# Kernel optimization log

Hardware: AMD Instinct MI355X
Metric: run time of the kernel (lower is better)

The kernel has to match this reference:

```python
import jax, jax.numpy as jnp
import numpy as np

B, P, D, H = 4, 2048, 768, 12
DFF = 4 * D
EPS = 1e-3  # Keras LayerNormalization default epsilon
SURVIVAL_PROB = 0.9  # inference-mode droppath scaling


def setup_inputs() -> dict:
    key = jax.random.key(0)
    ks = jax.random.split(key, 4)
    s = 0.02
    return {
        "x": jax.random.normal(ks[0], (B, P, D), dtype=jnp.float32),
        "ln1_g": jnp.ones((D,), jnp.float32),
        "ln1_b": jnp.zeros((D,), jnp.float32),
        "w_qkv": jax.random.normal(ks[1], (D, 3 * D), jnp.float32) * s,
        "b_qkv": jnp.zeros((3 * D,), jnp.float32),
        "ln2_g": jnp.ones((D,), jnp.float32),
        "ln2_b": jnp.zeros((D,), jnp.float32),
        "w1": jax.random.normal(ks[2], (D, DFF), jnp.float32) * s,
        "b1": jnp.zeros((DFF,), jnp.float32),
        "w2": jax.random.normal(ks[3], (DFF, D), jnp.float32) * s,
        "b2": jnp.zeros((D,), jnp.float32),
    }


def _layernorm(x, g, b):
    mu = jnp.mean(x, axis=-1, keepdims=True)
    var = jnp.mean(jnp.square(x - mu), axis=-1, keepdims=True)
    return (x - mu) * jax.lax.rsqrt(var + EPS) * g + b


def _block(x, ln1_g, ln1_b, w_qkv, b_qkv, ln2_g, ln2_b, w1, b1, w2, b2):
    # --- pre-norm self-attention ---
    h = _layernorm(x, ln1_g, ln1_b)
    qkv = h @ w_qkv + b_qkv                      # [B,P,3D]
    q, k, v = jnp.split(qkv, 3, axis=-1)
    hd = D // H
    to_heads = lambda t: t.reshape(B, P, H, hd).transpose(0, 2, 1, 3)  # b h p c
    q, k, v = to_heads(q), to_heads(k), to_heads(v)
    scale = jnp.sqrt(jnp.float32(D / H))
    scores = jnp.einsum('bhqc,bhkc->bhqk', q, k) / scale
    attn = jax.nn.softmax(scores, axis=-1)
    o = jnp.einsum('bhqk,bhkc->bhqc', attn, v)
    o = o.transpose(0, 2, 1, 3).reshape(B, P, D)
    x = o * SURVIVAL_PROB + x
    # --- pre-norm MLP ---
    h = _layernorm(x, ln2_g, ln2_b)
    h = jax.nn.gelu(h @ w1 + b1, approximate=False)
    h = h @ w2 + b2
    return h * SURVIVAL_PROB + x


def reference(x, ln1_g, ln1_b, w_qkv, b_qkv, ln2_g, ln2_b, w1, b1, w2, b2):
    return _block(x, ln1_g, ln1_b, w_qkv, b_qkv, ln2_g, ln2_b, w1, b1, w2, b2)
```

## Files before the change

kernel.cpp:

```cpp
#include <hip/hip_runtime.h>
#include <hip/hip_bf16.h>
#include <math.h>

#define B_ 4
#define P_ 2048
#define D_ 768
#define H_ 12

typedef __attribute__((ext_vector_type(8))) short bf16x8;
typedef __attribute__((ext_vector_type(4))) float f32x4;

static __device__ __forceinline__ short f2bf(float f) {
  union { float f; unsigned u; } z; z.f = f;
  unsigned r = z.u + 0x7fffu + ((z.u >> 16) & 1u);
  return (short)(r >> 16);
}

static __device__ __forceinline__ float bf2f(short s) {
  union { unsigned u; float f; } z;
  z.u = ((unsigned)(unsigned short)s) << 16;
  return z.f;
}

static __device__ __forceinline__ void gll16(const void* g, void* l) {
  __builtin_amdgcn_global_load_lds(
      (const __attribute__((address_space(1))) void*)g,
      (__attribute__((address_space(3))) void*)l, 16, 0, 0);
}

static __device__ __forceinline__ int vswz(int d) {
  return ((d & 7) ^ ((d >> 3) & 7)) << 3;
}

__global__ __launch_bounds__(256) void tcvt_kernel(const float* __restrict__ in,
                                                   short* __restrict__ out, int K, int N) {
  __shared__ float t[32][33];
  int k0 = blockIdx.x * 32, n0 = blockIdx.y * 32;
  int tx = threadIdx.x & 31, ty = threadIdx.x >> 5;
#pragma unroll
  for (int i = 0; i < 4; ++i)
    t[ty + 8 * i][tx] = in[(size_t)(k0 + ty + 8 * i) * N + n0 + tx];
  __syncthreads();
#pragma unroll
  for (int i = 0; i < 4; ++i)
    out[(size_t)(n0 + ty + 8 * i) * K + k0 + tx] = f2bf(t[tx][ty + 8 * i]);
}

__global__ __launch_bounds__(256) void ln_kernel(const float* __restrict__ in,
                                                 const float* __restrict__ g,
                                                 const float* __restrict__ be,
                                                 short* __restrict__ out) {
  int row = blockIdx.x, tid = threadIdx.x;
  const float* xr = in + (size_t)row * D_;
  float v0 = xr[tid], v1 = xr[tid + 256], v2 = xr[tid + 512];
  float s = v0 + v1 + v2;
  float ss = v0 * v0 + v1 * v1 + v2 * v2;
#pragma unroll
  for (int d = 1; d < 64; d <<= 1) {
    s += __shfl_xor(s, d, 64);
    ss += __shfl_xor(ss, d, 64);
  }
  __shared__ float red[8];
  int w = tid >> 6;
  if ((tid & 63) == 0) { red[w] = s; red[4 + w] = ss; }
  __syncthreads();
  s = red[0] + red[1] + red[2] + red[3];
  ss = red[4] + red[5] + red[6] + red[7];
  float mu = s * (1.0f / D_);
  float rstd = rsqrtf(ss * (1.0f / D_) - mu * mu + 1e-3f);
  short* orow = out + (size_t)row * D_;
  orow[tid]       = f2bf((v0 - mu) * rstd * g[tid]       + be[tid]);
  orow[tid + 256] = f2bf((v1 - mu) * rstd * g[tid + 256] + be[tid + 256]);
  orow[tid + 512] = f2bf((v2 - mu) * rstd * g[tid + 512] + be[tid + 512]);
}

template <int EPI>
__global__ __launch_bounds__(256, 3) void gemm128(
    const short* __restrict__ A, const short* __restrict__ Bt,
    const float* __restrict__ bias, short* __restrict__ out_bf,
    float* __restrict__ out_f, const float* __restrict__ resid,
    int M, int N, int K) {
  alignas(16) __shared__ short a_lds[128 * 32];
  alignas(16) __shared__ short b_lds[128 * 32];
  const int tid = threadIdx.x;
  const int wv = tid >> 6, lane = tid & 63;
  const int wm = wv >> 1, wn = wv & 1;
  const int g = lane >> 4, r = lane & 15;
  const int m0 = blockIdx.x * 128, n0 = blockIdx.y * 128;
  const int srow = lane >> 2, sseg = lane & 3;
  f32x4 acc[4][4] = {};
  const short* aptr = A + (size_t)(m0 + wv * 16 + srow) * K + sseg * 8;
  const short* bptr = Bt + (size_t)(n0 + wv * 16 + srow) * K + sseg * 8;
  short* alds0 = &a_lds[(wv * 16) * 32];
  short* blds0 = &b_lds[(wv * 16) * 32];
  for (int k0 = 0; k0 < K; k0 += 32) {
    __syncthreads();
    gll16(aptr + k0, alds0);
    gll16(aptr + k0 + (size_t)64 * K, alds0 + 64 * 32);
    gll16(bptr + k0, blds0);
    gll16(bptr + k0 + (size_t)64 * K, blds0 + 64 * 32);
    __syncthreads();
    bf16x8 af[4], bfr[4];
#pragma unroll
    for (int i = 0; i < 4; ++i)
      af[i] = *reinterpret_cast<const bf16x8*>(&a_lds[(wm * 64 + i * 16 + r) * 32 + g * 8]);
#pragma unroll
    for (int i = 0; i < 4; ++i)
      bfr[i] = *reinterpret_cast<const bf16x8*>(&b_lds[(wn * 64 + i * 16 + r) * 32 + g * 8]);
#pragma unroll
    for (int i = 0; i < 4; ++i)
#pragma unroll
      for (int jn = 0; jn < 4; ++jn)
        acc[i][jn] = __builtin_amdgcn_mfma_f32_16x16x32_bf16(af[i], bfr[jn], acc[i][jn], 0, 0, 0);
  }
#pragma unroll
  for (int i = 0; i < 4; ++i) {
#pragma unroll
    for (int jn = 0; jn < 4; ++jn) {
      int col = n0 + wn * 64 + jn * 16 + r;
      float bb = bias[col];
#pragma unroll
      for (int jj = 0; jj < 4; ++jj) {
        int row = m0 + wm * 64 + i * 16 + g * 4 + jj;
        float v = acc[i][jn][jj] + bb;
        size_t idx = (size_t)row * N + col;
        if (EPI == 0) {
          out_bf[idx] = f2bf(v);
        } else if (EPI == 1) {
          v = 0.5f * v * (1.0f + erff(v * 0.70710678118654752f));
          out_bf[idx] = f2bf(v);
        } else {
          out_f[idx] = v * 0.9f + resid[idx];
        }
      }
    }
  }
}

__global__ __launch_bounds__(256, 3) void attn_kernel(const short* __restrict__ qkv,
                                                      const float* __restrict__ x,
                                                      float* __restrict__ x2) {
  alignas(16) __shared__ short k_lds[64 * 72];
  alignas(16) __shared__ short vt_lds[64 * 64];
  alignas(16) __shared__ short p_lds[4][32 * 72];
  const int tid = threadIdx.x, wv = tid >> 6, lane = tid & 63;
  const int g = lane >> 4, r = lane & 15;
  const int b = blockIdx.y / H_, h = blockIdx.y % H_;
  const int TD = 3 * D_;
  const int qrow0 = blockIdx.x * 128 + wv * 32;
  bf16x8 qf[2][2];
#pragma unroll
  for (int mf = 0; mf < 2; ++mf)
#pragma unroll
    for (int kb = 0; kb < 2; ++kb) {
      bf16x8 q = *reinterpret_cast<const bf16x8*>(
          qkv + (size_t)(b * P_ + qrow0 + mf * 16 + r) * TD + h * 64 + kb * 32 + g * 8);
#pragma unroll
      for (int e = 0; e < 8; ++e) q[e] = f2bf(bf2f(q[e]) * 0.125f);
      qf[mf][kb] = q;
    }
  f32x4 acc[2][4] = {};
  float m_run[2], l_run[2];
#pragma unroll
  for (int mf = 0; mf < 2; ++mf) { m_run[mf] = -1e30f; l_run[mf] = 0.0f; }
  const int lrow = tid >> 2, lseg = tid & 3;
  short* p_w = &p_lds[wv][0];
  const int bcast = 20 * g;
  for (int kc = 0; kc < P_; kc += 64) {
    const short* src = qkv + (size_t)(b * P_ + kc + lrow) * TD + D_ + h * 64 + lseg * 16;
    bf16x8 kv0 = *reinterpret_cast<const bf16x8*>(src);
    bf16x8 kv1 = *reinterpret_cast<const bf16x8*>(src + 8);
    bf16x8 vv0 = *reinterpret_cast<const bf16x8*>(src + D_);
    bf16x8 vv1 = *reinterpret_cast<const bf16x8*>(src + D_ + 8);
    __syncthreads();
    *reinterpret_cast<bf16x8*>(&k_lds[lrow * 72 + lseg * 16]) = kv0;
    *reinterpret_cast<bf16x8*>(&k_lds[lrow * 72 + lseg * 16 + 8]) = kv1;
#pragma unroll
    for (int j = 0; j < 8; ++j) {
      int d0 = lseg * 16 + j, d1 = d0 + 8;
      vt_lds[d0 * 64 + (lrow ^ vswz(d0))] = vv0[j];
      vt_lds[d1 * 64 + (lrow ^ vswz(d1))] = vv1[j];
    }
    __syncthreads();
    f32x4 st[2][4];
#pragma unroll
    for (int cf = 0; cf < 4; ++cf) {
      bf16x8 kf0 = *reinterpret_cast<const bf16x8*>(&k_lds[(cf * 16 + r) * 72 + g * 8]);
      bf16x8 kf1 = *reinterpret_cast<const bf16x8*>(&k_lds[(cf * 16 + r) * 72 + 32 + g * 8]);
#pragma unroll
      for (int mf = 0; mf < 2; ++mf) {
        f32x4 s = {};
        s = __builtin_amdgcn_mfma_f32_16x16x32_bf16(kf0, qf[mf][0], s, 0, 0, 0);
        s = __builtin_amdgcn_mfma_f32_16x16x32_bf16(kf1, qf[mf][1], s, 0, 0, 0);
        st[mf][cf] = s;
      }
    }
#pragma unroll
    for (int mf = 0; mf < 2; ++mf) {
      float mx = st[mf][0][0];
#pragma unroll
      for (int cf = 0; cf < 4; ++cf)
#pragma unroll
        for (int j = 0; j < 4; ++j) mx = fmaxf(mx, st[mf][cf][j]);
      mx = fmaxf(mx, __shfl_xor(mx, 16, 64));
      mx = fmaxf(mx, __shfl_xor(mx, 32, 64));
      float mn = fmaxf(m_run[mf], mx);
      float corr = __expf(m_run[mf] - mn);
      m_run[mf] = mn;
      float p[4][4];
      float ls = 0.0f;
#pragma unroll
      for (int cf = 0; cf < 4; ++cf)
#pragma unroll
        for (int j = 0; j < 4; ++j) {
          float pv = __expf(st[mf][cf][j] - mn);
          p[cf][j] = pv;
          ls += pv;
        }
      ls += __shfl_xor(ls, 16, 64);
      ls += __shfl_xor(ls, 32, 64);
      l_run[mf] = l_run[mf] * corr + ls;
      short* prow = &p_w[(mf * 16 + r) * 72];
#pragma unroll
      for (int cf = 0; cf < 4; ++cf) {
        __hip_bfloat162 lo = __float22bfloat162_rn(make_float2(p[cf][0], p[cf][1]));
        __hip_bfloat162 hi = __float22bfloat162_rn(make_float2(p[cf][2], p[cf][3]));
        union { __hip_bfloat162 h2; unsigned u; } c0, c1;
        c0.h2 = lo; c1.h2 = hi;
        *reinterpret_cast<uint2*>(&prow[cf * 16 + 4 * g]) = make_uint2(c0.u, c1.u);
      }
      float cb0 = __shfl(corr, bcast + 0, 64);
      float cb1 = __shfl(corr, bcast + 1, 64);
      float cb2 = __shfl(corr, bcast + 2, 64);
      float cb3 = __shfl(corr, bcast + 3, 64);
#pragma unroll
      for (int cf = 0; cf < 4; ++cf) {
        acc[mf][cf][0] *= cb0; acc[mf][cf][1] *= cb1;
        acc[mf][cf][2] *= cb2; acc[mf][cf][3] *= cb3;
      }
    }
    bf16x8 vf[4][2];
#pragma unroll
    for (int cf = 0; cf < 4; ++cf) {
      int d = cf * 16 + r;
      int sw = vswz(d);
      vf[cf][0] = *reinterpret_cast<const bf16x8*>(&vt_lds[d * 64 + ((g * 8) ^ sw)]);
      vf[cf][1] = *reinterpret_cast<const bf16x8*>(&vt_lds[d * 64 + ((32 + g * 8) ^ sw)]);
    }
#pragma unroll
    for (int mf = 0; mf < 2; ++mf) {
      bf16x8 pf0 = *reinterpret_cast<const bf16x8*>(&p_w[(mf * 16 + r) * 72 + g * 8]);
      bf16x8 pf1 = *reinterpret_cast<const bf16x8*>(&p_w[(mf * 16 + r) * 72 + 32 + g * 8]);
#pragma unroll
      for (int cf = 0; cf < 4; ++cf) {
        acc[mf][cf] = __builtin_amdgcn_mfma_f32_16x16x32_bf16(pf0, vf[cf][0], acc[mf][cf], 0, 0, 0);
        acc[mf][cf] = __builtin_amdgcn_mfma_f32_16x16x32_bf16(pf1, vf[cf][1], acc[mf][cf], 0, 0, 0);
      }
    }
  }
#pragma unroll
  for (int mf = 0; mf < 2; ++mf) {
    float lb0 = 0.9f / __shfl(l_run[mf], bcast + 0, 64);
    float lb1 = 0.9f / __shfl(l_run[mf], bcast + 1, 64);
    float lb2 = 0.9f / __shfl(l_run[mf], bcast + 2, 64);
    float lb3 = 0.9f / __shfl(l_run[mf], bcast + 3, 64);
    float lb[4] = {lb0, lb1, lb2, lb3};
#pragma unroll
    for (int cf = 0; cf < 4; ++cf) {
      int col = h * 64 + cf * 16 + r;
#pragma unroll
      for (int j = 0; j < 4; ++j) {
        int row = qrow0 + mf * 16 + g * 4 + j;
        size_t idx = (size_t)(b * P_ + row) * D_ + col;
        x2[idx] = acc[mf][cf][j] * lb[j] + x[idx];
      }
    }
  }
}

extern "C" void kernel_launch(void* const* d_in, const int* in_sizes, int n_in,
                              void* d_out, int out_size, void* d_ws, size_t ws_size,
                              hipStream_t stream) {
  const float* x     = (const float*)d_in[0];
  const float* ln1_g = (const float*)d_in[1];
  const float* ln1_b = (const float*)d_in[2];
  const float* w_qkv = (const float*)d_in[3];
  const float* b_qkv = (const float*)d_in[4];
  const float* ln2_g = (const float*)d_in[5];
  const float* ln2_b = (const float*)d_in[6];
  const float* w1    = (const float*)d_in[7];
  const float* b1    = (const float*)d_in[8];
  const float* w2    = (const float*)d_in[9];
  const float* b2    = (const float*)d_in[10];
  float* out = (float*)d_out;
  char* ws = (char*)d_ws;

  short* wqkv_t = (short*)(ws);
  short* w1_t   = (short*)(ws + 3538944);
  short* w2_t   = (short*)(ws + 8257536);
  short* h_bf   = (short*)(ws + 12976128);
  short* qkv_bf = (short*)(ws + 25559040);
  short* a1_bf  = qkv_bf;

  const int R = B_ * P_;

  { dim3 g2(768 / 32, 2304 / 32);  tcvt_kernel<<<g2, 256, 0, stream>>>(w_qkv, wqkv_t, 768, 2304); }
  { dim3 g2(768 / 32, 3072 / 32);  tcvt_kernel<<<g2, 256, 0, stream>>>(w1, w1_t, 768, 3072); }
  { dim3 g2(3072 / 32, 768 / 32);  tcvt_kernel<<<g2, 256, 0, stream>>>(w2, w2_t, 3072, 768); }

  ln_kernel<<<R, 256, 0, stream>>>(x, ln1_g, ln1_b, h_bf);

  {
    dim3 grid(R / 128, 2304 / 128);
    gemm128<0><<<grid, 256, 0, stream>>>(h_bf, wqkv_t, b_qkv, qkv_bf, nullptr, nullptr,
                                         R, 2304, 768);
  }
  {
    dim3 grid(P_ / 128, B_ * H_);
    attn_kernel<<<grid, 256, 0, stream>>>(qkv_bf, x, out);
  }
  ln_kernel<<<R, 256, 0, stream>>>(out, ln2_g, ln2_b, h_bf);
  {
    dim3 grid(R / 128, 3072 / 128);
    gemm128<1><<<grid, 256, 0, stream>>>(h_bf, w1_t, b1, a1_bf, nullptr, nullptr,
                                         R, 3072, 768);
  }
  {
    dim3 grid(R / 128, 768 / 128);
    gemm128<2><<<grid, 256, 0, stream>>>(a1_bf, w2_t, b2, nullptr, out, out,
                                         R, 768, 3072);
  }
}
```

Before: 397.3 us.

## Double-buffer GEMM LDS tiles and skip softmax rescale when max barely grows

The GEMM kernel now holds two LDS buffers per operand and prefetches the next K tile while computing on the current one, so each iteration needs one barrier instead of two and global-to-LDS loads overlap the MFMAs. The flash attention loop applies the running-max correction (exp, shuffles, accumulator rescale) only when some lane's new max exceeds the stored max by more than 8. Otherwise it keeps the stale max, which saves work but lets exponentials reach up to e^8 before normalisation. Doubling LDS per GEMM block may lower occupancy under the 3-blocks-per-SM launch bound.

Result: no change. 400.3 us (+0.7%).

```diff
diff --git a/kernel.cpp b/kernel.cpp
--- a/kernel.cpp
+++ b/kernel.cpp
@@ -80,8 +80,8 @@
     const float* __restrict__ bias, short* __restrict__ out_bf,
     float* __restrict__ out_f, const float* __restrict__ resid,
     int M, int N, int K) {
-  alignas(16) __shared__ short a_lds[128 * 32];
-  alignas(16) __shared__ short b_lds[128 * 32];
+  alignas(16) __shared__ short a_lds[2][128 * 32];
+  alignas(16) __shared__ short b_lds[2][128 * 32];
   const int tid = threadIdx.x;
   const int wv = tid >> 6, lane = tid & 63;
   const int wm = wv >> 1, wn = wv & 1;
@@ -91,27 +91,39 @@
   f32x4 acc[4][4] = {};
   const short* aptr = A + (size_t)(m0 + wv * 16 + srow) * K + sseg * 8;
   const short* bptr = Bt + (size_t)(n0 + wv * 16 + srow) * K + sseg * 8;
-  short* alds0 = &a_lds[(wv * 16) * 32];
-  short* blds0 = &b_lds[(wv * 16) * 32];
-  for (int k0 = 0; k0 < K; k0 += 32) {
-    __syncthreads();
-    gll16(aptr + k0, alds0);
-    gll16(aptr + k0 + (size_t)64 * K, alds0 + 64 * 32);
-    gll16(bptr + k0, blds0);
-    gll16(bptr + k0 + (size_t)64 * K, blds0 + 64 * 32);
-    __syncthreads();
+  const int aoff = (wv * 16) * 32;
+
+  gll16(aptr, &a_lds[0][aoff]);
+  gll16(aptr + (size_t)64 * K, &a_lds[0][aoff + 64 * 32]);
+  gll16(bptr, &b_lds[0][aoff]);
+  gll16(bptr + (size_t)64 * K, &b_lds[0][aoff + 64 * 32]);
+  __syncthreads();
+
+  const int nt = K / 32;
+  int cur = 0;
+  for (int t = 0; t < nt; ++t) {
+    if (t + 1 < nt) {
+      const int k0 = (t + 1) * 32;
+      const int nb = cur ^ 1;
+      gll16(aptr + k0, &a_lds[nb][aoff]);
+      gll16(aptr + k0 + (size_t)64 * K, &a_lds[nb][aoff + 64 * 32]);
+      gll16(bptr + k0, &b_lds[nb][aoff]);
+      gll16(bptr + k0 + (size_t)64 * K, &b_lds[nb][aoff + 64 * 32]);
+    }
     bf16x8 af[4], bfr[4];
 #pragma unroll
     for (int i = 0; i < 4; ++i)
-      af[i] = *reinterpret_cast<const bf16x8*>(&a_lds[(wm * 64 + i * 16 + r) * 32 + g * 8]);
+      af[i] = *reinterpret_cast<const bf16x8*>(&a_lds[cur][(wm * 64 + i * 16 + r) * 32 + g * 8]);
 #pragma unroll
     for (int i = 0; i < 4; ++i)
-      bfr[i] = *reinterpret_cast<const bf16x8*>(&b_lds[(wn * 64 + i * 16 + r) * 32 + g * 8]);
+      bfr[i] = *reinterpret_cast<const bf16x8*>(&b_lds[cur][(wn * 64 + i * 16 + r) * 32 + g * 8]);
 #pragma unroll
     for (int i = 0; i < 4; ++i)
 #pragma unroll
       for (int jn = 0; jn < 4; ++jn)
         acc[i][jn] = __builtin_amdgcn_mfma_f32_16x16x32_bf16(af[i], bfr[jn], acc[i][jn], 0, 0, 0);
+    __syncthreads();
+    cur ^= 1;
   }
 #pragma unroll
   for (int i = 0; i < 4; ++i) {
@@ -204,9 +216,22 @@
         for (int j = 0; j < 4; ++j) mx = fmaxf(mx, st[mf][cf][j]);
       mx = fmaxf(mx, __shfl_xor(mx, 16, 64));
       mx = fmaxf(mx, __shfl_xor(mx, 32, 64));
-      float mn = fmaxf(m_run[mf], mx);
-      float corr = __expf(m_run[mf] - mn);
-      m_run[mf] = mn;
+      if (!__all(mx - m_run[mf] <= 8.0f)) {
+        float mn = fmaxf(m_run[mf], mx);
+        float corr = __expf(m_run[mf] - mn);
+        m_run[mf] = mn;
+        l_run[mf] *= corr;
+        float cb0 = __shfl(corr, bcast + 0, 64);
+        float cb1 = __shfl(corr, bcast + 1, 64);
+        float cb2 = __shfl(corr, bcast + 2, 64);
+        float cb3 = __shfl(corr, bcast + 3, 64);
+#pragma unroll
+        for (int cf = 0; cf < 4; ++cf) {
+          acc[mf][cf][0] *= cb0; acc[mf][cf][1] *= cb1;
+          acc[mf][cf][2] *= cb2; acc[mf][cf][3] *= cb3;
+        }
+      }
+      float mn = m_run[mf];
       float p[4][4];
       float ls = 0.0f;
 #pragma unroll
@@ -219,7 +244,7 @@
         }
       ls += __shfl_xor(ls, 16, 64);
       ls += __shfl_xor(ls, 32, 64);
-      l_run[mf] = l_run[mf] * corr + ls;
+      l_run[mf] += ls;
       short* prow = &p_w[(mf * 16 + r) * 72];
 #pragma unroll
       for (int cf = 0; cf < 4; ++cf) {
@@ -228,15 +253,6 @@
         union { __hip_bfloat162 h2; unsigned u; } c0, c1;
         c0.h2 = lo; c1.h2 = hi;
         *reinterpret_cast<uint2*>(&prow[cf * 16 + 4 * g]) = make_uint2(c0.u, c1.u);
-      }
-      float cb0 = __shfl(corr, bcast + 0, 64);
-      float cb1 = __shfl(corr, bcast + 1, 64);
-      float cb2 = __shfl(corr, bcast + 2, 64);
-      float cb3 = __shfl(corr, bcast + 3, 64);
-#pragma unroll
-      for (int cf = 0; cf < 4; ++cf) {
-        acc[mf][cf][0] *= cb0; acc[mf][cf][1] *= cb1;
-        acc[mf][cf][2] *= cb2; acc[mf][cf][3] *= cb3;
       }
     }
     bf16x8 vf[4][2];
```

## Double-buffer GEMM LDS tiles with prefetch two stages ahead and XOR swizzle

Applied to the files above, without the earlier changes.

The GEMM main loop now keeps two LDS buffers and issues global-to-LDS loads for tile t+2 while computing tile t, using explicit vmcnt waits and raw barriers instead of two __syncthreads per iteration. It also XOR-swizzles the 16-byte segment index within each row to reduce LDS bank conflicts on fragment reads. LDS use doubles, which may limit occupancy at the 3-blocks launch bound, and the hand-placed waitcnt and barrier logic is fragile.

Result: faster. 388.5 us (-2.2%).

```diff
diff --git a/kernel.cpp b/kernel.cpp
--- a/kernel.cpp
+++ b/kernel.cpp
@@ -80,8 +80,8 @@
     const float* __restrict__ bias, short* __restrict__ out_bf,
     float* __restrict__ out_f, const float* __restrict__ resid,
     int M, int N, int K) {
-  alignas(16) __shared__ short a_lds[128 * 32];
-  alignas(16) __shared__ short b_lds[128 * 32];
+  alignas(16) __shared__ short a_lds[2][128 * 32];
+  alignas(16) __shared__ short b_lds[2][128 * 32];
   const int tid = threadIdx.x;
   const int wv = tid >> 6, lane = tid & 63;
   const int wm = wv >> 1, wn = wv & 1;
@@ -89,29 +89,54 @@
   const int m0 = blockIdx.x * 128, n0 = blockIdx.y * 128;
   const int srow = lane >> 2, sseg = lane & 3;
   f32x4 acc[4][4] = {};
-  const short* aptr = A + (size_t)(m0 + wv * 16 + srow) * K + sseg * 8;
-  const short* bptr = Bt + (size_t)(n0 + wv * 16 + srow) * K + sseg * 8;
-  short* alds0 = &a_lds[(wv * 16) * 32];
-  short* blds0 = &b_lds[(wv * 16) * 32];
-  for (int k0 = 0; k0 < K; k0 += 32) {
-    __syncthreads();
-    gll16(aptr + k0, alds0);
-    gll16(aptr + k0 + (size_t)64 * K, alds0 + 64 * 32);
-    gll16(bptr + k0, blds0);
-    gll16(bptr + k0 + (size_t)64 * K, blds0 + 64 * 32);
-    __syncthreads();
+  const int sw_seg = sseg ^ (srow & 3);
+  const short* aptr = A + (size_t)(m0 + wv * 16 + srow) * K + sw_seg * 8;
+  const short* bptr = Bt + (size_t)(n0 + wv * 16 + srow) * K + sw_seg * 8;
+  const int aoff = (wv * 16) * 32;
+
+  auto stage = [&](int k0, int buf) {
+    gll16(aptr + k0, &a_lds[buf][aoff]);
+    gll16(aptr + k0 + (size_t)64 * K, &a_lds[buf][aoff + 64 * 32]);
+    gll16(bptr + k0, &b_lds[buf][aoff]);
+    gll16(bptr + k0 + (size_t)64 * K, &b_lds[buf][aoff + 64 * 32]);
+  };
+
+  const int nt = K / 32;
+  stage(0, 0);
+  stage(32, 1);
+  asm volatile("s_waitcnt vmcnt(4)" ::: "memory");
+  __builtin_amdgcn_s_barrier();
+  __builtin_amdgcn_sched_barrier(0);
+
+  for (int t = 0; t < nt; ++t) {
+    const int cur = t & 1;
     bf16x8 af[4], bfr[4];
 #pragma unroll
     for (int i = 0; i < 4; ++i)
-      af[i] = *reinterpret_cast<const bf16x8*>(&a_lds[(wm * 64 + i * 16 + r) * 32 + g * 8]);
+      af[i] = *reinterpret_cast<const bf16x8*>(
+          &a_lds[cur][(wm * 64 + i * 16 + r) * 32 + ((g ^ (r & 3)) * 8)]);
 #pragma unroll
     for (int i = 0; i < 4; ++i)
-      bfr[i] = *reinterpret_cast<const bf16x8*>(&b_lds[(wn * 64 + i * 16 + r) * 32 + g * 8]);
+      bfr[i] = *reinterpret_cast<const bf16x8*>(
+          &b_lds[cur][(wn * 64 + i * 16 + r) * 32 + ((g ^ (r & 3)) * 8)]);
+    asm volatile("s_waitcnt lgkmcnt(0)" ::: "memory");
+    __builtin_amdgcn_sched_barrier(0);
+    __builtin_amdgcn_s_barrier();
+    __builtin_amdgcn_sched_barrier(0);
+    if (t + 2 < nt) stage((t + 2) * 32, cur);
 #pragma unroll
     for (int i = 0; i < 4; ++i)
 #pragma unroll
       for (int jn = 0; jn < 4; ++jn)
         acc[i][jn] = __builtin_amdgcn_mfma_f32_16x16x32_bf16(af[i], bfr[jn], acc[i][jn], 0, 0, 0);
+    if (t + 1 < nt) {
+      if (t + 2 < nt)
+        asm volatile("s_waitcnt vmcnt(4)" ::: "memory");
+      else
+        asm volatile("s_waitcnt vmcnt(0)" ::: "memory");
+      __builtin_amdgcn_s_barrier();
+      __builtin_amdgcn_sched_barrier(0);
+    }
   }
 #pragma unroll
   for (int i = 0; i < 4; ++i) {
```
